# Performance work log

Hardware: AMD Instinct MI355X
Metric: run time of the kernel (lower is better)

The kernel has to match this reference:

```python
import jax, jax.numpy as jnp
import numpy as np

B, P, DV, DT, E, A, K = 256, 192, 768, 768, 256, 8, 4


def _l2n(x):
    return x / jnp.maximum(jnp.linalg.norm(x, axis=-1, keepdims=True), 1e-12)


def _hungarian_min(cost):
    """Jonker-Volgenant style Hungarian (e-maxx formulation), minimizes cost.
    cost: [n, m] with n <= m. Returns (row_ind, col_ind) like scipy's
    linear_sum_assignment."""
    cost = np.asarray(cost, dtype=np.float64)
    n, m = cost.shape
    INF = 1e18
    u = np.zeros(n + 1)
    v = np.zeros(m + 1)
    p = np.zeros(m + 1, dtype=np.int64)   # p[j] = row matched to col j (1-based)
    way = np.zeros(m + 1, dtype=np.int64)
    for i in range(1, n + 1):
        p[0] = i
        j0 = 0
        minv = np.full(m + 1, INF)
        used = np.zeros(m + 1, dtype=bool)
        while True:
            used[j0] = True
            i0 = p[j0]
            cur = cost[i0 - 1] - u[i0] - v[1:]
            free = ~used[1:]
            better = free & (cur < minv[1:])
            minv[1:][better] = cur[better]
            way[1:][better] = j0
            cand = np.where(free, minv[1:], INF)
            j1 = int(np.argmin(cand)) + 1
            delta = cand[j1 - 1]
            u[p[used]] += delta
            v[used] -= delta
            minv[1:][free] -= delta
            j0 = j1
            if p[j0] == 0:
                break
        while j0 != 0:
            j1 = way[j0]
            p[j0] = p[j1]
            j0 = j1
    rows = p[1:]
    cols = np.arange(m)
    sel = rows != 0
    rows = rows[sel] - 1
    cols = cols[sel]
    order = np.argsort(rows)
    return rows[order], cols[order]


def _topk_assign_indices(sim_np, k):
    """Replicates get_topk_assign_similarity's iterative masked re-assignment,
    returning per-round match indices. sim_np: [B, A, P] numpy."""
    b_, a_, _ = sim_np.shape
    rows = np.zeros((k, b_, a_), dtype=np.int64)
    cols = np.zeros((k, b_, a_), dtype=np.int64)
    for b in range(b_):
        mat = sim_np[b].copy()
        for r in range(k):
            ri, ci = _hungarian_min(-mat)  # maximize similarity
            rows[r, b] = ri
            cols[r, b] = ci
            mat[ri, ci] = -100.0
        # (host loop over small per-sample Hungarian solves; this is exactly
        #  the serialized pattern the original module exhibits)
    return rows, cols


def setup_inputs() -> dict:
    key = jax.random.key(0)
    ks = jax.random.split(key, 8)
    s = (2.0 / E) ** 0.5  # kaiming_normal fan_out on [E, in] torch weight
    return {
        "visual_feature": jax.random.normal(ks[0], (B, 1 + P, DV), jnp.float32),
        "textual_feature": jax.random.normal(ks[1], (B, DT), jnp.float32),
        "attribute_feature": jax.random.normal(ks[2], (B * A, DT), jnp.float32),
        "att_nums": jnp.full((B,), A, dtype=jnp.int32),
        "Wv": jax.random.normal(ks[3], (DV, E), jnp.float32) * s,
        "bv": jnp.zeros((E,), jnp.float32),
        "Wt": jax.random.normal(ks[4], (DT, E), jnp.float32) * s,
        "bt": jnp.zeros((E,), jnp.float32),
        "Wp": jax.random.normal(ks[5], (DV, E), jnp.float32) * s,
        "bp": jnp.zeros((E,), jnp.float32),
        "Wa": jax.random.normal(ks[6], (DT, E), jnp.float32) * s,
        "ba": jnp.zeros((E,), jnp.float32),
    }


def reference(visual_feature, textual_feature, attribute_feature, att_nums,
              Wv, bv, Wt, bt, Wp, bp, Wa, ba):
    # ViT path: avgpool is None; split CLS token / patch tokens
    visual_embed = visual_feature[:, 0] @ Wv + bv            # [B, E]
    textual_embed = textual_feature @ Wt + bt                # [B, E]
    patch_embed = visual_feature[:, 1:] @ Wp + bp            # [B, P, E]
    att_embed = attribute_feature @ Wa + ba                  # [B*A, E]

    # get_local_similarity: L2-normalize then per-sample sim matrices.
    # att_nums is constant A per sample, so the ragged slicing is a reshape.
    att = _l2n(att_embed).reshape(B, A, E)
    pat = _l2n(patch_embed)
    sim = jnp.einsum('bae,bpe->bap', att, pat)               # [B, A, P]

    # Hungarian assignment on detached values (torch: .detach().cpu())
    rows, cols = _topk_assign_indices(np.asarray(sim), K)
    rows = jnp.asarray(rows)
    cols = jnp.asarray(cols)

    bidx = jnp.arange(B)[:, None]
    sim_m = sim
    total = jnp.zeros((B,), sim.dtype)
    for r in range(K):
        total = total + sim_m[bidx, rows[r], cols[r]].mean(-1)
        sim_m = sim_m.at[bidx, rows[r], cols[r]].set(-100.0)
    local_similarity = total / K                              # [B]

    return (visual_embed, textual_embed, local_similarity)
```

## Files before the change

### kernel.cpp

```cpp
#include <hip/hip_runtime.h>
#include <hip/hip_bf16.h>

typedef float f32x4 __attribute__((ext_vector_type(4)));
typedef short s16x8 __attribute__((ext_vector_type(8)));

__device__ __forceinline__ unsigned short f2bf(float f) {
  unsigned int x = __builtin_bit_cast(unsigned int, f);
  x += 0x7fffu + ((x >> 16) & 1u);
  return (unsigned short)(x >> 16);
}
__device__ __forceinline__ float bf2f(unsigned short u) {
  return __builtin_bit_cast(float, ((unsigned int)u) << 16);
}
__device__ __forceinline__ unsigned int packbf(float lo, float hi) {
  return (unsigned int)f2bf(lo) | ((unsigned int)f2bf(hi) << 16);
}
__device__ __forceinline__ void mfma16(f32x4& acc, s16x8 a, s16x8 b) {
  asm volatile("v_mfma_f32_16x16x32_bf16 %0, %1, %2, %0"
               : "+v"(acc)
               : "v"(a), "v"(b));
}
__device__ __forceinline__ void gload_lds16(const void* g, void* l) {
  __builtin_amdgcn_global_load_lds(
      (const __attribute__((address_space(1))) unsigned int*)g,
      (__attribute__((address_space(3))) unsigned int*)l, 16, 0, 0);
}

__global__ __launch_bounds__(256) void prep_wt(const float* __restrict__ W,
                                               unsigned short* __restrict__ Wt) {
  int i = blockIdx.x * 256 + threadIdx.x;
  int k = i >> 8, col = i & 255;
  int kt = k >> 5, kl = k & 31;
  unsigned off = (unsigned)((col * 64 + kl * 2) ^ ((col & 3) << 4));
  Wt[(unsigned)(kt * 16384 + off) >> 1] = f2bf(W[i]);
}

__global__ __launch_bounds__(512, 2) void patch_gemm(
    const float* __restrict__ vf, const unsigned short* __restrict__ Wt,
    const float* __restrict__ bias, unsigned short* __restrict__ patch) {
  __shared__ char lds[57344];
  __shared__ float rssq[192];

  const int tid = threadIdx.x;
  const int lane = tid & 63, wid = tid >> 6;
  const int wm = wid >> 2, wn = wid & 3;
  const int l15 = lane & 15, l4 = lane >> 4;
  const int blk = blockIdx.x;

  if (tid < 192) rssq[tid] = 0.f;

  const float* Ag = vf + ((size_t)blk * 193 + 1) * 768;

  f32x4 acc[6][4] = {};
  f32x4 areg[3];

  auto stageA_load = [&](int kt) {
#pragma unroll
    for (int c = 0; c < 3; ++c) {
      int idx4 = c * 512 + tid;
      int row = idx4 >> 3, k4 = (idx4 & 7) * 4;
      areg[c] = *(const f32x4*)(Ag + (size_t)row * 768 + kt * 32 + k4);
    }
  };
  auto stageA_write = [&](int buf) {
#pragma unroll
    for (int c = 0; c < 3; ++c) {
      int idx4 = c * 512 + tid;
      int row = idx4 >> 3, k4 = (idx4 & 7) * 4;
      unsigned off = (unsigned)((row * 64 + k4 * 2) ^ ((row & 3) << 4));
      uint2 u;
      u.x = packbf(areg[c].x, areg[c].y);
      u.y = packbf(areg[c].z, areg[c].w);
      *(uint2*)(lds + buf * 12288 + off) = u;
    }
  };
  auto stageB = [&](int kt, int buf) {
#pragma unroll
    for (int it = 0; it < 2; ++it) {
      int off = wid * 2048 + it * 1024;
      gload_lds16((const char*)Wt + kt * 16384 + off + lane * 16,
                  lds + 24576 + buf * 16384 + off);
    }
  };
  auto compute = [&](int buf) {
    const char* Ab = lds + buf * 12288;
    const char* Bb = lds + 24576 + buf * 16384;
    const int kb = l4 * 16;
    s16x8 af[6];
#pragma unroll
    for (int mf = 0; mf < 6; ++mf) {
      int row = wm * 96 + mf * 16 + l15;
      unsigned off = (unsigned)((row * 64 + kb) ^ ((row & 3) << 4));
      af[mf] = *(const s16x8*)(Ab + off);
    }
    s16x8 bfr[4];
#pragma unroll
    for (int nf = 0; nf < 4; ++nf) {
      int col = wn * 64 + nf * 16 + l15;
      unsigned off = (unsigned)((col * 64 + kb) ^ ((col & 3) << 4));
      bfr[nf] = *(const s16x8*)(Bb + off);
    }
#pragma unroll
    for (int mf = 0; mf < 6; ++mf)
#pragma unroll
      for (int nf = 0; nf < 4; ++nf) mfma16(acc[mf][nf], af[mf], bfr[nf]);
  };

  stageA_load(0);
  stageB(0, 0);
  stageA_write(0);
  __syncthreads();

  int cur = 0;
  for (int kt = 0; kt < 24; ++kt) {
    if (kt < 23) {
      stageA_load(kt + 1);
      stageB(kt + 1, cur ^ 1);
    }
    compute(cur);
    if (kt < 23) stageA_write(cur ^ 1);
    __syncthreads();
    cur ^= 1;
  }

  __builtin_amdgcn_sched_barrier(0);
  asm volatile("s_nop 7\n\ts_nop 7");
  __builtin_amdgcn_sched_barrier(0);

  float bcol[4];
#pragma unroll
  for (int nf = 0; nf < 4; ++nf) bcol[nf] = bias[wn * 64 + nf * 16 + l15];
#pragma unroll
  for (int mf = 0; mf < 6; ++mf)
#pragma unroll
    for (int nf = 0; nf < 4; ++nf)
#pragma unroll
      for (int j = 0; j < 4; ++j) acc[mf][nf][j] += bcol[nf];

#pragma unroll
  for (int mf = 0; mf < 6; ++mf)
#pragma unroll
    for (int j = 0; j < 4; ++j) {
      float p = 0.f;
#pragma unroll
      for (int nf = 0; nf < 4; ++nf) {
        float v = acc[mf][nf][j];
        p += v * v;
      }
#pragma unroll
      for (int m = 1; m < 16; m <<= 1) p += __shfl_xor(p, m);
      if (l15 == 0) atomicAdd(&rssq[wm * 96 + mf * 16 + l4 * 4 + j], p);
    }
  __syncthreads();

  unsigned short* outp = patch + (size_t)blk * 192 * 256;
#pragma unroll
  for (int mf = 0; mf < 6; ++mf)
#pragma unroll
    for (int j = 0; j < 4; ++j) {
      int row = wm * 96 + mf * 16 + l4 * 4 + j;
      float scale = 1.f / fmaxf(sqrtf(rssq[row]), 1e-12f);
#pragma unroll
      for (int nf = 0; nf < 4; ++nf) {
        int col = wn * 64 + nf * 16 + l15;
        outp[(size_t)row * 256 + col] = f2bf(acc[mf][nf][j] * scale);
      }
    }
}

__global__ __launch_bounds__(256) void vt_gemm(
    const float* __restrict__ vf, const float* __restrict__ tf,
    const float* __restrict__ Wv, const float* __restrict__ bv,
    const float* __restrict__ Wtx, const float* __restrict__ bt,
    float* __restrict__ out) {
  __shared__ float As[32][33];
  __shared__ float Bs[32][68];
  const bool vis = blockIdx.y < 8;
  const int row0 = (vis ? blockIdx.y : blockIdx.y - 8) * 32;
  const int col0 = blockIdx.x * 64;
  const float* A = vis ? vf : tf;
  const float* W = vis ? Wv : Wtx;
  const float* bias = vis ? bv : bt;
  float* C = vis ? out : out + 65536;
  const size_t rstride = vis ? (size_t)193 * 768 : (size_t)768;

  const int tid = threadIdx.x;
  const int tx = tid & 15, ty = tid >> 4;
  const int lr = tid >> 3, lk = (tid & 7) * 4;
  const float* Arow = A + (size_t)(row0 + lr) * rstride;
  const int bk = tid >> 4, bn = (tid & 15) * 4;
  const float* Wp = W + (size_t)bk * 256 + col0 + bn;
  float acc[2][4] = {};

  for (int k0 = 0; k0 < 768; k0 += 32) {
    float4 a0 = *(const float4*)(Arow + k0 + lk);
    float4 b0 = *(const float4*)(Wp + (size_t)k0 * 256);
    float4 b1 = *(const float4*)(Wp + (size_t)(k0 + 16) * 256);
    __syncthreads();
    As[lk + 0][lr] = a0.x; As[lk + 1][lr] = a0.y;
    As[lk + 2][lr] = a0.z; As[lk + 3][lr] = a0.w;
    *(float4*)&Bs[bk][bn] = b0;
    *(float4*)&Bs[bk + 16][bn] = b1;
    __syncthreads();
#pragma unroll
    for (int k = 0; k < 32; ++k) {
      float a0v = As[k][ty * 2], a1v = As[k][ty * 2 + 1];
      float4 bv4 = *(const float4*)&Bs[k][tx * 4];
      acc[0][0] += a0v * bv4.x; acc[0][1] += a0v * bv4.y;
      acc[0][2] += a0v * bv4.z; acc[0][3] += a0v * bv4.w;
      acc[1][0] += a1v * bv4.x; acc[1][1] += a1v * bv4.y;
      acc[1][2] += a1v * bv4.z; acc[1][3] += a1v * bv4.w;
    }
  }
  float4 b4 = *(const float4*)(bias + col0 + tx * 4);
#pragma unroll
  for (int i = 0; i < 2; ++i) {
    int r = row0 + ty * 2 + i;
    float4 o;
    o.x = acc[i][0] + b4.x; o.y = acc[i][1] + b4.y;
    o.z = acc[i][2] + b4.z; o.w = acc[i][3] + b4.w;
    *(float4*)(C + (size_t)r * 256 + col0 + tx * 4) = o;
  }
}

__global__ __launch_bounds__(256) void att_gemm(
    const float* __restrict__ A, const float* __restrict__ W,
    const float* __restrict__ bias, float* __restrict__ C) {
  __shared__ float As[32][33];
  __shared__ float Bs[32][68];
  const int tid = threadIdx.x;
  const int row0 = blockIdx.y * 32, col0 = blockIdx.x * 64;
  const int tx = tid & 15, ty = tid >> 4;
  const int lr = tid >> 3, lk = (tid & 7) * 4;
  const float* Arow = A + (size_t)(row0 + lr) * 768;
  const int bk = tid >> 4, bn = (tid & 15) * 4;
  const float* Wp = W + (size_t)bk * 256 + col0 + bn;
  float acc[2][4] = {};

  for (int k0 = 0; k0 < 768; k0 += 32) {
    float4 a0 = *(const float4*)(Arow + k0 + lk);
    float4 b0 = *(const float4*)(Wp + (size_t)k0 * 256);
    float4 b1 = *(const float4*)(Wp + (size_t)(k0 + 16) * 256);
    __syncthreads();
    As[lk + 0][lr] = a0.x; As[lk + 1][lr] = a0.y;
    As[lk + 2][lr] = a0.z; As[lk + 3][lr] = a0.w;
    *(float4*)&Bs[bk][bn] = b0;
    *(float4*)&Bs[bk + 16][bn] = b1;
    __syncthreads();
#pragma unroll
    for (int k = 0; k < 32; ++k) {
      float a0v = As[k][ty * 2], a1v = As[k][ty * 2 + 1];
      float4 bv4 = *(const float4*)&Bs[k][tx * 4];
      acc[0][0] += a0v * bv4.x; acc[0][1] += a0v * bv4.y;
      acc[0][2] += a0v * bv4.z; acc[0][3] += a0v * bv4.w;
      acc[1][0] += a1v * bv4.x; acc[1][1] += a1v * bv4.y;
      acc[1][2] += a1v * bv4.z; acc[1][3] += a1v * bv4.w;
    }
  }
  float4 b4 = *(const float4*)(bias + col0 + tx * 4);
#pragma unroll
  for (int i = 0; i < 2; ++i) {
    int r = row0 + ty * 2 + i;
    float4 o;
    o.x = acc[i][0] + b4.x; o.y = acc[i][1] + b4.y;
    o.z = acc[i][2] + b4.z; o.w = acc[i][3] + b4.w;
    *(float4*)(C + (size_t)r * 256 + col0 + tx * 4) = o;
  }
}

__global__ __launch_bounds__(256) void l2norm_kernel(float* __restrict__ X,
                                                     int rows) {
  int row = blockIdx.x * 4 + (threadIdx.x >> 6);
  int lane = threadIdx.x & 63;
  if (row >= rows) return;
  float4* px = (float4*)(X + (size_t)row * 256);
  float4 v = px[lane];
  float ss = v.x * v.x + v.y * v.y + v.z * v.z + v.w * v.w;
#pragma unroll
  for (int off = 1; off < 64; off <<= 1) ss += __shfl_xor(ss, off);
  float n = fmaxf(sqrtf(ss), 1e-12f);
  v.x /= n; v.y /= n; v.z /= n; v.w /= n;
  px[lane] = v;
}

__global__ __launch_bounds__(192) void sim_kernel(
    const float* __restrict__ att, const unsigned short* __restrict__ pat,
    float* __restrict__ sim) {
  const int b = blockIdx.x;
  __shared__ float attS[8][256];
  const int tid = threadIdx.x;
  for (int idx = tid; idx < 2048; idx += 192)
    ((float*)attS)[idx] = att[(size_t)b * 2048 + idx];
  __syncthreads();

  const unsigned short* prow = pat + ((size_t)b * 192 + tid) * 256;
  float acc[8] = {};
  for (int e8 = 0; e8 < 32; ++e8) {
    uint4 pv = *(const uint4*)(prow + e8 * 8);
    float f[8];
    f[0] = bf2f((unsigned short)(pv.x & 0xffff)); f[1] = bf2f((unsigned short)(pv.x >> 16));
    f[2] = bf2f((unsigned short)(pv.y & 0xffff)); f[3] = bf2f((unsigned short)(pv.y >> 16));
    f[4] = bf2f((unsigned short)(pv.z & 0xffff)); f[5] = bf2f((unsigned short)(pv.z >> 16));
    f[6] = bf2f((unsigned short)(pv.w & 0xffff)); f[7] = bf2f((unsigned short)(pv.w >> 16));
#pragma unroll
    for (int a = 0; a < 8; ++a) {
      const float* ap = &attS[a][e8 * 8];
#pragma unroll
      for (int i = 0; i < 8; ++i) acc[a] += f[i] * ap[i];
    }
  }
#pragma unroll
  for (int a = 0; a < 8; ++a)
    sim[(size_t)b * 1536 + a * 192 + tid] = acc[a];
}

__global__ __launch_bounds__(64) void hungarian_kernel(
    const float* __restrict__ sim, float* __restrict__ out) {
  const int b = blockIdx.x;
  const int lane = threadIdx.x;
  __shared__ int p[193];
  __shared__ int way[193];

  float Sr[8][3];
  const float* simb = sim + (size_t)b * 1536;
#pragma unroll
  for (int r = 0; r < 8; ++r)
#pragma unroll
    for (int c = 0; c < 3; ++c) Sr[r][c] = simb[r * 192 + c * 64 + lane];

  double total = 0.0;

  for (int round = 0; round < 4; ++round) {
    for (int idx = lane; idx < 193; idx += 64) p[idx] = 0;
    double u1 = 0, u2 = 0, u3 = 0, u4 = 0, u5 = 0, u6 = 0, u7 = 0, u8 = 0;
    double v0 = 0.0, v1 = 0.0, v2 = 0.0;
    int pc0 = 0, pc1 = 0, pc2 = 0;
    __syncthreads();

    for (int i = 1; i <= 8; ++i) {
      if (lane == 0) p[0] = i;
      double m0 = 1e18, m1 = 1e18, m2 = 1e18;
      int used = 0;
      int j0 = 0;
      int pj0 = i;
      int rowmask = 0;

      while (true) {
        rowmask |= 1 << pj0;
        if (j0 != 0 && ((j0 - 1) & 63) == lane) used |= 1 << ((j0 - 1) >> 6);
        const int i0 = __builtin_amdgcn_readfirstlane(pj0);

        double ui0 = u1;
        if (i0 == 2) ui0 = u2;
        if (i0 == 3) ui0 = u3;
        if (i0 == 4) ui0 = u4;
        if (i0 == 5) ui0 = u5;
        if (i0 == 6) ui0 = u6;
        if (i0 == 7) ui0 = u7;
        if (i0 == 8) ui0 = u8;

        float s0 = Sr[0][0], s1 = Sr[0][1], s2 = Sr[0][2];
#pragma unroll
        for (int r = 1; r < 8; ++r)
          if (i0 == r + 1) { s0 = Sr[r][0]; s1 = Sr[r][1]; s2 = Sr[r][2]; }

        double bestv = 1e18;
        int bestj = 0x7fffffff;
        int bestpj = 0;
        if (!(used & 1)) {
          double cur = -(double)s0 - ui0 - v0;
          if (cur < m0) { m0 = cur; way[1 + lane] = j0; }
          if (m0 < bestv) { bestv = m0; bestj = 1 + lane; bestpj = pc0; }
        }
        if (!(used & 2)) {
          double cur = -(double)s1 - ui0 - v1;
          if (cur < m1) { m1 = cur; way[65 + lane] = j0; }
          if (m1 < bestv) { bestv = m1; bestj = 65 + lane; bestpj = pc1; }
        }
        if (!(used & 4)) {
          double cur = -(double)s2 - ui0 - v2;
          if (cur < m2) { m2 = cur; way[129 + lane] = j0; }
          if (m2 < bestv) { bestv = m2; bestj = 129 + lane; bestpj = pc2; }
        }
#pragma unroll
        for (int off = 1; off < 64; off <<= 1) {
          double ov = __shfl_xor(bestv, off);
          int oj = __shfl_xor(bestj, off);
          int opj = __shfl_xor(bestpj, off);
          if (ov < bestv || (ov == bestv && oj < bestj)) {
            bestv = ov; bestj = oj; bestpj = opj;
          }
        }
        const double delta = bestv;

        if (rowmask & (1 << 1)) u1 += delta;
        if (rowmask & (1 << 2)) u2 += delta;
        if (rowmask & (1 << 3)) u3 += delta;
        if (rowmask & (1 << 4)) u4 += delta;
        if (rowmask & (1 << 5)) u5 += delta;
        if (rowmask & (1 << 6)) u6 += delta;
        if (rowmask & (1 << 7)) u7 += delta;
        if (rowmask & (1 << 8)) u8 += delta;
        if (used & 1) v0 -= delta; else m0 -= delta;
        if (used & 2) v1 -= delta; else m1 -= delta;
        if (used & 4) v2 -= delta; else m2 -= delta;

        j0 = bestj;
        pj0 = bestpj;
        if (pj0 == 0) break;
      }

      __syncthreads();
      if (lane == 0) {
        int j = j0;
        while (j != 0) {
          int jp = way[j];
          p[j] = p[jp];
          j = jp;
        }
      }
      __syncthreads();
      pc0 = p[1 + lane];
      pc1 = p[65 + lane];
      pc2 = p[129 + lane];
    }

    double s = 0.0;
    if (pc0) {
#pragma unroll
      for (int r = 0; r < 8; ++r)
        if (pc0 == r + 1) { s += (double)Sr[r][0]; Sr[r][0] = -100.f; }
    }
    if (pc1) {
#pragma unroll
      for (int r = 0; r < 8; ++r)
        if (pc1 == r + 1) { s += (double)Sr[r][1]; Sr[r][1] = -100.f; }
    }
    if (pc2) {
#pragma unroll
      for (int r = 0; r < 8; ++r)
        if (pc2 == r + 1) { s += (double)Sr[r][2]; Sr[r][2] = -100.f; }
    }
#pragma unroll
    for (int off = 1; off < 64; off <<= 1) s += __shfl_xor(s, off);
    total += s;
    __syncthreads();
  }

  if (lane == 0) out[b] = (float)(total * (1.0 / 32.0));
}

extern "C" void kernel_launch(void* const* d_in, const int* in_sizes, int n_in,
                              void* d_out, int out_size, void* d_ws,
                              size_t ws_size, hipStream_t stream) {
  const float* vf = (const float*)d_in[0];
  const float* tf = (const float*)d_in[1];
  const float* af = (const float*)d_in[2];
  const float* Wv = (const float*)d_in[4];
  const float* bv = (const float*)d_in[5];
  const float* Wtx = (const float*)d_in[6];
  const float* bt = (const float*)d_in[7];
  const float* Wp = (const float*)d_in[8];
  const float* bp = (const float*)d_in[9];
  const float* Wa = (const float*)d_in[10];
  const float* ba = (const float*)d_in[11];

  float* out = (float*)d_out;
  float* visual_out = out;
  float* ls_out = out + 131072;

  char* ws = (char*)d_ws;
  unsigned short* patch = (unsigned short*)ws;
  float* attE = (float*)(ws + (size_t)25165824);
  float* sim = (float*)(ws + (size_t)25165824 + 2097152);
  unsigned short* Wt_s = (unsigned short*)(ws + (size_t)25165824 + 2097152 + 1572864);

  prep_wt<<<768, 256, 0, stream>>>(Wp, Wt_s);

  vt_gemm<<<dim3(4, 16), 256, 0, stream>>>(vf, tf, Wv, bv, Wtx, bt, visual_out);

  att_gemm<<<dim3(4, 64), 256, 0, stream>>>(af, Wa, ba, attE);

  l2norm_kernel<<<512, 256, 0, stream>>>(attE, 2048);

  patch_gemm<<<256, 512, 0, stream>>>(vf, Wt_s, bp, patch);

  sim_kernel<<<256, 192, 0, stream>>>(attE, patch, sim);

  hungarian_kernel<<<256, 64, 0, stream>>>(sim, ls_out);
}
```

Measured before the change: 384.1 us.

## Fuse attribute GEMM, L2 norm and similarity into one per-sample kernel

Replaces the separate att_gemm, l2norm and sim_kernel launches with a single kernel per sample. The kernel computes the 8 attribute embeddings with a split-K reduction in shared memory, normalizes them, then computes the similarities with one wave per patch row and shuffle reductions. This removes two launches and the global round trip of the attribute embeddings. In exchange each block rereads all of Wa, the fused GEMM runs on only 256 blocks, and the shuffle-heavy dot products may cost more than the old per-thread loop.

```diff
diff --git a/kernel.cpp b/kernel.cpp
--- a/kernel.cpp
+++ b/kernel.cpp
@@ -9,8 +9,8 @@
   x += 0x7fffu + ((x >> 16) & 1u);
   return (unsigned short)(x >> 16);
 }
-__device__ __forceinline__ float bf2f(unsigned short u) {
-  return __builtin_bit_cast(float, ((unsigned int)u) << 16);
+__device__ __forceinline__ float bf2f(unsigned int u) {
+  return __builtin_bit_cast(float, (u & 0xffffu) << 16);
 }
 __device__ __forceinline__ unsigned int packbf(float lo, float hi) {
   return (unsigned int)f2bf(lo) | ((unsigned int)f2bf(hi) << 16);
@@ -223,95 +223,106 @@
   }
 }
 
-__global__ __launch_bounds__(256) void att_gemm(
-    const float* __restrict__ A, const float* __restrict__ W,
-    const float* __restrict__ bias, float* __restrict__ C) {
-  __shared__ float As[32][33];
-  __shared__ float Bs[32][68];
-  const int tid = threadIdx.x;
-  const int row0 = blockIdx.y * 32, col0 = blockIdx.x * 64;
-  const int tx = tid & 15, ty = tid >> 4;
-  const int lr = tid >> 3, lk = (tid & 7) * 4;
-  const float* Arow = A + (size_t)(row0 + lr) * 768;
-  const int bk = tid >> 4, bn = (tid & 15) * 4;
-  const float* Wp = W + (size_t)bk * 256 + col0 + bn;
-  float acc[2][4] = {};
-
-  for (int k0 = 0; k0 < 768; k0 += 32) {
-    float4 a0 = *(const float4*)(Arow + k0 + lk);
-    float4 b0 = *(const float4*)(Wp + (size_t)k0 * 256);
-    float4 b1 = *(const float4*)(Wp + (size_t)(k0 + 16) * 256);
-    __syncthreads();
-    As[lk + 0][lr] = a0.x; As[lk + 1][lr] = a0.y;
-    As[lk + 2][lr] = a0.z; As[lk + 3][lr] = a0.w;
-    *(float4*)&Bs[bk][bn] = b0;
-    *(float4*)&Bs[bk + 16][bn] = b1;
-    __syncthreads();
-#pragma unroll
-    for (int k = 0; k < 32; ++k) {
-      float a0v = As[k][ty * 2], a1v = As[k][ty * 2 + 1];
-      float4 bv4 = *(const float4*)&Bs[k][tx * 4];
-      acc[0][0] += a0v * bv4.x; acc[0][1] += a0v * bv4.y;
-      acc[0][2] += a0v * bv4.z; acc[0][3] += a0v * bv4.w;
-      acc[1][0] += a1v * bv4.x; acc[1][1] += a1v * bv4.y;
-      acc[1][2] += a1v * bv4.z; acc[1][3] += a1v * bv4.w;
-    }
-  }
-  float4 b4 = *(const float4*)(bias + col0 + tx * 4);
-#pragma unroll
-  for (int i = 0; i < 2; ++i) {
-    int r = row0 + ty * 2 + i;
-    float4 o;
-    o.x = acc[i][0] + b4.x; o.y = acc[i][1] + b4.y;
-    o.z = acc[i][2] + b4.z; o.w = acc[i][3] + b4.w;
-    *(float4*)(C + (size_t)r * 256 + col0 + tx * 4) = o;
-  }
-}
-
-__global__ __launch_bounds__(256) void l2norm_kernel(float* __restrict__ X,
-                                                     int rows) {
-  int row = blockIdx.x * 4 + (threadIdx.x >> 6);
-  int lane = threadIdx.x & 63;
-  if (row >= rows) return;
-  float4* px = (float4*)(X + (size_t)row * 256);
-  float4 v = px[lane];
-  float ss = v.x * v.x + v.y * v.y + v.z * v.z + v.w * v.w;
-#pragma unroll
-  for (int off = 1; off < 64; off <<= 1) ss += __shfl_xor(ss, off);
-  float n = fmaxf(sqrtf(ss), 1e-12f);
-  v.x /= n; v.y /= n; v.z /= n; v.w /= n;
-  px[lane] = v;
-}
-
-__global__ __launch_bounds__(192) void sim_kernel(
-    const float* __restrict__ att, const unsigned short* __restrict__ pat,
+__global__ __launch_bounds__(512, 2) void simatt(
+    const float* __restrict__ af, const float* __restrict__ Wa,
+    const float* __restrict__ ba, const unsigned short* __restrict__ pat,
     float* __restrict__ sim) {
   const int b = blockIdx.x;
-  __shared__ float attS[8][256];
   const int tid = threadIdx.x;
-  for (int idx = tid; idx < 2048; idx += 192)
-    ((float*)attS)[idx] = att[(size_t)b * 2048 + idx];
-  __syncthreads();
-
-  const unsigned short* prow = pat + ((size_t)b * 192 + tid) * 256;
-  float acc[8] = {};
-  for (int e8 = 0; e8 < 32; ++e8) {
-    uint4 pv = *(const uint4*)(prow + e8 * 8);
-    float f[8];
-    f[0] = bf2f((unsigned short)(pv.x & 0xffff)); f[1] = bf2f((unsigned short)(pv.x >> 16));
-    f[2] = bf2f((unsigned short)(pv.y & 0xffff)); f[3] = bf2f((unsigned short)(pv.y >> 16));
-    f[4] = bf2f((unsigned short)(pv.z & 0xffff)); f[5] = bf2f((unsigned short)(pv.z >> 16));
-    f[6] = bf2f((unsigned short)(pv.w & 0xffff)); f[7] = bf2f((unsigned short)(pv.w >> 16));
-#pragma unroll
-    for (int a = 0; a < 8; ++a) {
-      const float* ap = &attS[a][e8 * 8];
-#pragma unroll
-      for (int i = 0; i < 8; ++i) acc[a] += f[i] * ap[i];
-    }
-  }
-#pragma unroll
-  for (int a = 0; a < 8; ++a)
-    sim[(size_t)b * 1536 + a * 192 + tid] = acc[a];
+  const int lane = tid & 63, wid = tid >> 6;
+
+  __shared__ float af_s[8][768];
+  __shared__ float part[8][8][256];
+  __shared__ float att_s[8][256];
+  __shared__ float rnorm_s[8];
+
+#pragma unroll
+  for (int c = 0; c < 3; ++c) {
+    int idx = c * 512 + tid;
+    int row = idx / 192, k4 = (idx % 192) * 4;
+    *(float4*)&af_s[row][k4] =
+        *(const float4*)(af + ((size_t)(b * 8 + row)) * 768 + k4);
+  }
+  __syncthreads();
+
+  {
+    const int c0 = lane * 4;
+    const int kbase = wid * 96;
+    float pacc[8][4] = {};
+    for (int kk = 0; kk < 96; kk += 4) {
+      int k = kbase + kk;
+      float4 w0 = *(const float4*)(Wa + (size_t)(k + 0) * 256 + c0);
+      float4 w1 = *(const float4*)(Wa + (size_t)(k + 1) * 256 + c0);
+      float4 w2 = *(const float4*)(Wa + (size_t)(k + 2) * 256 + c0);
+      float4 w3 = *(const float4*)(Wa + (size_t)(k + 3) * 256 + c0);
+#pragma unroll
+      for (int a = 0; a < 8; ++a) {
+        float4 a4 = *(const float4*)&af_s[a][k];
+        pacc[a][0] += a4.x * w0.x + a4.y * w1.x + a4.z * w2.x + a4.w * w3.x;
+        pacc[a][1] += a4.x * w0.y + a4.y * w1.y + a4.z * w2.y + a4.w * w3.y;
+        pacc[a][2] += a4.x * w0.z + a4.y * w1.z + a4.z * w2.z + a4.w * w3.z;
+        pacc[a][3] += a4.x * w0.w + a4.y * w1.w + a4.z * w2.w + a4.w * w3.w;
+      }
+    }
+#pragma unroll
+    for (int a = 0; a < 8; ++a) *(float4*)&part[wid][a][c0] = *(float4*)pacc[a];
+  }
+  __syncthreads();
+
+  {
+    int c = tid & 255;
+    int ah = (tid >> 8) * 4;
+#pragma unroll
+    for (int q = 0; q < 4; ++q) {
+      int a = ah + q;
+      float e = ba[c];
+#pragma unroll
+      for (int w = 0; w < 8; ++w) e += part[w][a][c];
+      att_s[a][c] = e;
+    }
+  }
+  __syncthreads();
+
+  {
+    float4 v = *(const float4*)&att_s[wid][lane * 4];
+    float ss = v.x * v.x + v.y * v.y + v.z * v.z + v.w * v.w;
+#pragma unroll
+    for (int m = 1; m < 64; m <<= 1) ss += __shfl_xor(ss, m);
+    if (lane == 0) rnorm_s[wid] = 1.f / fmaxf(sqrtf(ss), 1e-12f);
+  }
+  __syncthreads();
+
+  float attreg[8][4];
+#pragma unroll
+  for (int a = 0; a < 8; ++a) {
+    float4 v = *(const float4*)&att_s[a][lane * 4];
+    float rn = rnorm_s[a];
+    attreg[a][0] = v.x * rn; attreg[a][1] = v.y * rn;
+    attreg[a][2] = v.z * rn; attreg[a][3] = v.w * rn;
+  }
+
+  const unsigned short* patb = pat + (size_t)b * 192 * 256;
+  float* simb = sim + (size_t)b * 1536;
+  for (int pr = 0; pr < 24; ++pr) {
+    int prow = wid * 24 + pr;
+    uint2 pv = *(const uint2*)(patb + (size_t)prow * 256 + lane * 4);
+    float f0 = bf2f(pv.x), f1 = bf2f(pv.x >> 16);
+    float f2 = bf2f(pv.y), f3 = bf2f(pv.y >> 16);
+    float acc[8];
+#pragma unroll
+    for (int a = 0; a < 8; ++a)
+      acc[a] = f0 * attreg[a][0] + f1 * attreg[a][1] +
+               f2 * attreg[a][2] + f3 * attreg[a][3];
+#pragma unroll
+    for (int a = 0; a < 8; ++a)
+#pragma unroll
+      for (int m = 1; m < 64; m <<= 1) acc[a] += __shfl_xor(acc[a], m);
+    float sel = acc[0];
+#pragma unroll
+    for (int a = 1; a < 8; ++a)
+      if (lane == a) sel = acc[a];
+    if (lane < 8) simb[lane * 192 + prow] = sel;
+  }
 }
 
 __global__ __launch_bounds__(64) void hungarian_kernel(
@@ -471,21 +482,16 @@
 
   char* ws = (char*)d_ws;
   unsigned short* patch = (unsigned short*)ws;
-  float* attE = (float*)(ws + (size_t)25165824);
-  float* sim = (float*)(ws + (size_t)25165824 + 2097152);
-  unsigned short* Wt_s = (unsigned short*)(ws + (size_t)25165824 + 2097152 + 1572864);
+  unsigned short* Wt_s = (unsigned short*)(ws + (size_t)25165824);
+  float* sim = (float*)(ws + (size_t)25165824 + 393216);
 
   prep_wt<<<768, 256, 0, stream>>>(Wp, Wt_s);
 
   vt_gemm<<<dim3(4, 16), 256, 0, stream>>>(vf, tf, Wv, bv, Wtx, bt, visual_out);
 
-  att_gemm<<<dim3(4, 64), 256, 0, stream>>>(af, Wa, ba, attE);
-
-  l2norm_kernel<<<512, 256, 0, stream>>>(attE, 2048);
-
   patch_gemm<<<256, 512, 0, stream>>>(vf, Wt_s, bp, patch);
 
-  sim_kernel<<<256, 192, 0, stream>>>(attE, patch, sim);
+  simatt<<<256, 512, 0, stream>>>(af, Wa, ba, patch, sim);
 
   hungarian_kernel<<<256, 64, 0, stream>>>(sim, ls_out);
 }
```

Result: no change. 383.3 us (-0.2%).
